# Performance work log

Hardware: AMD Instinct MI355X
Metric: run time of the kernel (lower is better)

The kernel has to match this reference:

```python
import jax, jax.numpy as jnp
import numpy as np

NX, NY, NZ = 432, 496, 1
D = 64        # num_pt_features
K = 3         # NUM_K
M = 1024      # memory size
BEV = 128     # num_bev_features
NCOORD = 3
NV = 10000    # pillars in scene
NP = 16384    # points in scene
BN_EPS = 1e-3
SHRINK = 0.0025


def hard_shrink_relu(x, lambd, eps=1e-12):
    return jax.nn.relu(x - lambd) * x / (jnp.abs(x - lambd) + eps)


def batchnorm_train(x, gamma, beta, eps=BN_EPS):
    # torch BatchNorm1d training-mode math (biased variance)
    mu = jnp.mean(x, axis=0)
    var = jnp.mean((x - mu) ** 2, axis=0)
    return (x - mu) * jax.lax.rsqrt(var + eps) * gamma + beta


def pdist2(a, b, eps=1e-5):
    # sqrt(eps + |  ||a||^2 + ||b||^2 - 2 a.b |), shape [n1, n2]
    n1 = jnp.sum(a * a, axis=1, keepdims=True)
    n2 = jnp.sum(b * b, axis=1, keepdims=True)
    d2 = n1 + n2.T - 2.0 * (a @ b.T)
    return jnp.sqrt(eps + jnp.abs(d2))


def memory_lookup(x_flat, mem_w, shrink):
    # MemAE-style memory unit: softmax addressing + hard shrink + L1 renorm
    att = jax.nn.softmax(x_flat @ mem_w.T, axis=1)          # [N, M]
    att = hard_shrink_relu(att, shrink)
    att = att / jnp.maximum(jnp.sum(jnp.abs(att), axis=1, keepdims=True), 1e-12)
    return att @ mem_w                                       # [N, D]


def setup_inputs() -> dict:
    key = jax.random.key(0)
    ks = jax.random.split(key, 8)
    rng = np.random.default_rng(0)
    flat = rng.choice(NX * NY, size=NV, replace=False)       # unique BEV cells
    x = (flat % NX).astype(np.int32)
    y = (flat // NX).astype(np.int32)
    coords = jnp.asarray(np.stack([np.zeros(NV, np.int32), x, y,
                                   np.zeros(NV, np.int32)], axis=1))  # (b, x, y, z)
    pc = jax.random.uniform(ks[1], (NP, 4), dtype=jnp.float32)
    point_coords = pc * jnp.array([0.0, NX, NY, 1.0], dtype=jnp.float32)
    return {
        "pillar_features": jax.random.normal(ks[0], (NV, D), dtype=jnp.float32),
        "coords": coords,
        "point_features": jax.random.normal(ks[2], (NP, D), dtype=jnp.float32),
        "point_coords": point_coords,
        "adapt_w": jax.random.normal(ks[3], (BEV // 2, D * K), dtype=jnp.float32) * 0.05,
        "bn1_g": jnp.ones((BEV // 2,), dtype=jnp.float32),
        "bn1_b": jnp.zeros((BEV // 2,), dtype=jnp.float32),
        "weight_w": jax.random.normal(ks[4], (2, BEV // 2), dtype=jnp.float32) * 0.1,
        "bn2_g": jnp.ones((2,), dtype=jnp.float32),
        "bn2_b": jnp.zeros((2,), dtype=jnp.float32),
        "mem_w": jax.random.normal(ks[5], (M, D), dtype=jnp.float32) * 0.1,
    }


def reference(pillar_features, coords, point_features, point_coords,
              adapt_w, bn1_g, bn1_b, weight_w, bn2_g, bn2_b, mem_w):
    nv = pillar_features.shape[0]
    pillars = pillar_features.T                              # [D, nv]

    # --- coord-based retrieval: smallest-K pdist(pillar coords, point coords) ---
    dist = pdist2(coords.astype(jnp.float32), point_coords)  # [nv, np]
    _, idx_c = jax.lax.top_k(-dist, K)                       # [nv, K]
    pillars_positive_coord = point_features[idx_c]           # [nv, K, D]

    # --- feature-based retrieval: top-K of softmax(points @ pillars, axis=0) ---
    score = jax.nn.softmax(point_features @ pillars, axis=0) # [np, nv]
    _, idx_f = jax.lax.top_k(score.T, K)                     # [nv, K]
    points_positive = point_features[idx_f]                  # [nv, K, D]

    # --- memory unit on both branches ---
    out_f = memory_lookup(points_positive.reshape(nv * K, D), mem_w, SHRINK).reshape(nv, K * D)
    out_c = memory_lookup(pillars_positive_coord.reshape(nv * K, D), mem_w, SHRINK).reshape(nv, K * D)

    f = jax.nn.relu(batchnorm_train(out_f @ adapt_w.T, bn1_g, bn1_b))  # [nv, 64]
    c = jax.nn.relu(batchnorm_train(out_c @ adapt_w.T, bn1_g, bn1_b))  # [nv, 64]
    w = jax.nn.softmax(batchnorm_train(pillar_features @ weight_w.T, bn2_g, bn2_b), axis=-1)
    pillars_aug = w[:, :1] * f + w[:, 1:2] * c               # [nv, 64]
    pillars_full = jnp.concatenate([pillars, pillars_aug.T], axis=0)  # [128, nv]

    # --- scatter to BEV canvas ---
    bev_idx = coords[:, 1] + coords[:, 2] * NX + coords[:, 3]
    spatial = jnp.zeros((BEV, NX * NY), dtype=pillar_features.dtype).at[:, bev_idx].set(pillars_full)
    pind = jnp.zeros((NCOORD, NX * NY), dtype=pillar_features.dtype)
    pind = pind.at[0, bev_idx].set(coords[:, 2].astype(jnp.float32))
    pind = pind.at[1, bev_idx].set(coords[:, 3].astype(jnp.float32))
    pind = pind.at[2, bev_idx].set(coords[:, 1].astype(jnp.float32))

    spatial_features = spatial.reshape(1, BEV * NZ, NY, NX)
    spatial_indices = pind.reshape(1, NCOORD * NZ, NY, NX)
    return spatial_features, spatial_indices
```

## Files before the change

kernel.cpp:

```cpp
#include <hip/hip_runtime.h>
#include <math.h>

#define NXc 432
#define NYc 496
#define NVc 10000
#define NPc 16384
#define CELLS (NXc*NYc)
#define SHRINKc 0.0025f
#define NVPAD 10048
#define NBX 27
#define NBY 31
#define NBIN (NBX*NBY)

typedef unsigned short u16;
typedef __attribute__((ext_vector_type(8))) short s16x8;
typedef __attribute__((ext_vector_type(4))) float f32x4;

__device__ __forceinline__ unsigned med3u(unsigned a, unsigned b, unsigned c) {
    unsigned d;
    asm("v_med3_u32 %0, %1, %2, %3" : "=v"(d) : "v"(a), "v"(b), "v"(c));
    return d;
}

__device__ __forceinline__ u16 f2b(float x) {
    unsigned u = __float_as_uint(x);
    unsigned r = (u + 0x7fffu + ((u >> 16) & 1u)) >> 16;
    return (u16)r;
}

__global__ __launch_bounds__(256) void k_init(const float* __restrict__ pillar,
                                              const float* __restrict__ pfeat,
                                              const float* __restrict__ memw,
                                              const float* __restrict__ adapt,
                                              float* __restrict__ stats,
                                              int* __restrict__ cellMap,
                                              u16* __restrict__ pillarH,
                                              u16* __restrict__ pfeatH,
                                              u16* __restrict__ memwH,
                                              u16* __restrict__ memwTH,
                                              u16* __restrict__ badaptH) {
    int gid = blockIdx.x * 256 + threadIdx.x;
    if (gid < CELLS) cellMap[gid] = -1;
    if (gid < 260) stats[gid] = 0.f;
    const int N1 = NVPAD * 64;
    const int N2 = N1 + NPc * 64;
    const int N3 = N2 + 65536;
    const int N4 = N3 + 65536;
    if (gid < N1) {
        int v = gid >> 6;
        pillarH[gid] = f2b(v < NVc ? pillar[gid] : 0.f);
    } else if (gid < N2) {
        pfeatH[gid - N1] = f2b(pfeat[gid - N1]);
    } else if (gid < N3) {
        memwH[gid - N2] = f2b(memw[gid - N2]);
    } else if (gid < N4) {
        int i = gid - N3;
        int d = i >> 10, j = i & 1023;
        memwTH[i] = f2b(memw[j * 64 + d]);
    } else {
        int i = gid - N4;
        int c = i >> 6, d = i & 63;
        badaptH[i] = f2b(adapt[(c & 63) * 192 + (c >> 6) * 64 + d]);
    }
}

__global__ __launch_bounds__(1024) void k_pre(const float* __restrict__ pcoord,
                                              int* __restrict__ binStart,
                                              float4* __restrict__ binPC) {
    __shared__ int hcnt[1024];
    __shared__ int sc[1024];
    __shared__ int cur[1024];
    int t = threadIdx.x;
    hcnt[t] = 0;
    __syncthreads();
    for (int j = t; j < NPc; j += 1024) {
        float qx = pcoord[j * 4 + 1], qy = pcoord[j * 4 + 2];
        int bx = (int)(qx * 0.0625f); if (bx > NBX - 1) bx = NBX - 1;
        int by = (int)(qy * 0.0625f); if (by > NBY - 1) by = NBY - 1;
        atomicAdd(&hcnt[by * NBX + bx], 1);
    }
    __syncthreads();
    int vcount = (t < NBIN) ? hcnt[t] : 0;
    sc[t] = vcount;
    __syncthreads();
    for (int off = 1; off < 1024; off <<= 1) {
        int add = (t >= off) ? sc[t - off] : 0;
        __syncthreads();
        sc[t] += add;
        __syncthreads();
    }
    int excl = sc[t] - vcount;
    cur[t] = excl;
    if (t <= NBIN) binStart[t] = excl;
    __syncthreads();
    for (int j = t; j < NPc; j += 1024) {
        float qx = pcoord[j * 4 + 1], qy = pcoord[j * 4 + 2], qz = pcoord[j * 4 + 3];
        int bx = (int)(qx * 0.0625f); if (bx > NBX - 1) bx = NBX - 1;
        int by = (int)(qy * 0.0625f); if (by > NBY - 1) by = NBY - 1;
        int slot = atomicAdd(&cur[by * NBX + bx], 1);
        binPC[slot] = make_float4(qx, qy, qz * qz, __uint_as_float((unsigned)j));
    }
}

__global__ __launch_bounds__(256) void k_fused(const u16* __restrict__ pillarH,
                                               const u16* __restrict__ pfeatH,
                                               const u16* __restrict__ memwH,
                                               const u16* __restrict__ memwTH,
                                               const int* __restrict__ coords,
                                               const float4* __restrict__ binPC,
                                               const int* __restrict__ binStart,
                                               u16* __restrict__ PoutH,
                                               int* __restrict__ dIdx6,
                                               int* __restrict__ sIdx) {
    __shared__ union {
        u16 bf[2][8192];
        struct { u16 wh[4096]; u16 wt[4096]; u16 st[4][1024]; } m;
    } smem;
    int bid = blockIdx.x;
    int t = threadIdx.x;
    int w = t >> 6, l = t & 63;
    int lm = l & 15, qd = l >> 4;

    if (bid < 256) {
        int pb = bid * 64;
        u16* WH = smem.m.wh;
        u16* WT = smem.m.wt;
        u16* ST = &smem.m.st[w][0];
        const u16* arow = pfeatH + (size_t)(pb + 16 * w + lm) * 64 + qd * 8;
        s16x8 a0 = *(const s16x8*)arow;
        s16x8 a1 = *(const s16x8*)(arow + 32);
        float mM[4] = {-INFINITY, -INFINITY, -INFINITY, -INFINITY};
        float Zs[4] = {0.f, 0.f, 0.f, 0.f};
        for (int tile = 0; tile < 16; ++tile) {
            __syncthreads();
#pragma unroll
            for (int r = 0; r < 2; ++r) {
                int q = t + 256 * r;
                int row = q >> 3, g = q & 7;
                uint4 v = *(const uint4*)(memwH + (size_t)(tile * 64 + row) * 64 + g * 8);
                *(uint4*)&WH[(((row >> 4) * 8 + g) * 16 + ((row & 15) ^ g)) * 8] = v;
            }
            __syncthreads();
            f32x4 acc[4];
#pragma unroll
            for (int st = 0; st < 4; ++st) {
                s16x8 b0 = *(const s16x8*)&WH[((st * 8 + qd) * 16 + (lm ^ qd)) * 8];
                s16x8 b1 = *(const s16x8*)&WH[((st * 8 + qd + 4) * 16 + (lm ^ (qd + 4))) * 8];
                f32x4 z = {0.f, 0.f, 0.f, 0.f};
                z = __builtin_amdgcn_mfma_f32_16x16x32_bf16(a0, b0, z, 0, 0, 0);
                z = __builtin_amdgcn_mfma_f32_16x16x32_bf16(a1, b1, z, 0, 0, 0);
                acc[st] = z;
            }
#pragma unroll
            for (int r = 0; r < 4; ++r) {
                float tmax = acc[0][r];
#pragma unroll
                for (int st = 1; st < 4; ++st) tmax = fmaxf(tmax, acc[st][r]);
                float mn = fmaxf(mM[r], tmax);
                float zacc = Zs[r] * __expf(mM[r] - mn);
#pragma unroll
                for (int st = 0; st < 4; ++st) zacc += __expf(acc[st][r] - mn);
                mM[r] = mn; Zs[r] = zacc;
            }
        }
#pragma unroll
        for (int r = 0; r < 4; ++r) {
#pragma unroll
            for (int off = 1; off < 16; off <<= 1) {
                float om = __shfl_xor(mM[r], off);
                float oz = __shfl_xor(Zs[r], off);
                float mn = fmaxf(mM[r], om);
                Zs[r] = Zs[r] * __expf(mM[r] - mn) + oz * __expf(om - mn);
                mM[r] = mn;
            }
        }
        float invZ[4], L1[4] = {0.f, 0.f, 0.f, 0.f};
#pragma unroll
        for (int r = 0; r < 4; ++r) invZ[r] = 1.f / Zs[r];
        f32x4 oacc[4];
#pragma unroll
        for (int n = 0; n < 4; ++n) oacc[n] = (f32x4){0.f, 0.f, 0.f, 0.f};
        for (int tile = 0; tile < 16; ++tile) {
            __syncthreads();
#pragma unroll
            for (int r = 0; r < 2; ++r) {
                int q = t + 256 * r;
                int row = q >> 3, g = q & 7;
                uint4 v = *(const uint4*)(memwH + (size_t)(tile * 64 + row) * 64 + g * 8);
                *(uint4*)&WH[(((row >> 4) * 8 + g) * 16 + ((row & 15) ^ g)) * 8] = v;
            }
#pragma unroll
            for (int r = 0; r < 2; ++r) {
                int q = t + 256 * r;
                int row = q >> 3, g = q & 7;
                uint4 v = *(const uint4*)(memwTH + (size_t)row * 1024 + tile * 64 + g * 8);
                *(uint4*)&WT[(g * 64 + (row ^ g)) * 8] = v;
            }
            __syncthreads();
#pragma unroll
            for (int st = 0; st < 4; ++st) {
                s16x8 b0 = *(const s16x8*)&WH[((st * 8 + qd) * 16 + (lm ^ qd)) * 8];
                s16x8 b1 = *(const s16x8*)&WH[((st * 8 + qd + 4) * 16 + (lm ^ (qd + 4))) * 8];
                f32x4 z = {0.f, 0.f, 0.f, 0.f};
                z = __builtin_amdgcn_mfma_f32_16x16x32_bf16(a0, b0, z, 0, 0, 0);
                z = __builtin_amdgcn_mfma_f32_16x16x32_bf16(a1, b1, z, 0, 0, 0);
                int g2 = st * 2 + (lm >> 3);
#pragma unroll
                for (int r = 0; r < 4; ++r) {
                    float e = __expf(z[r] - mM[r]);
                    float a = e * invZ[r];
                    float tt = a - SHRINKc;
                    float sres = fmaxf(tt, 0.f) * a / (fabsf(tt) + 1e-12f);
                    L1[r] += sres;
                    int rr = qd * 4 + r;
                    ST[(g2 * 16 + (rr ^ g2)) * 8 + (lm & 7)] = f2b(sres);
                }
            }
#pragma unroll
            for (int ks = 0; ks < 2; ++ks) {
                int g = ks * 4 + qd;
                s16x8 af = *(const s16x8*)&ST[(g * 16 + (lm ^ g)) * 8];
#pragma unroll
                for (int n = 0; n < 4; ++n) {
                    s16x8 bf = *(const s16x8*)&WT[(g * 64 + ((n * 16 + lm) ^ g)) * 8];
                    oacc[n] = __builtin_amdgcn_mfma_f32_16x16x32_bf16(af, bf, oacc[n], 0, 0, 0);
                }
            }
        }
#pragma unroll
        for (int r = 0; r < 4; ++r) {
#pragma unroll
            for (int off = 1; off < 16; off <<= 1) L1[r] += __shfl_xor(L1[r], off);
            L1[r] = 1.f / fmaxf(L1[r], 1e-12f);
        }
#pragma unroll
        for (int n = 0; n < 4; ++n)
#pragma unroll
            for (int r = 0; r < 4; ++r)
                PoutH[(size_t)(pb + 16 * w + qd * 4 + r) * 64 + n * 16 + lm] =
                    f2b(oacc[n][r] * L1[r]);
    } else if (bid < 296) {
        int v = (bid - 256) * 256 + t;
        if (v >= NVc) return;
        int xi = coords[v * 4 + 1], yi = coords[v * 4 + 2];
        float x = (float)xi, y = (float)yi;
        int bx = xi >> 4; if (bx > NBX - 1) bx = NBX - 1;
        int by = yi >> 4; if (by > NBY - 1) by = NBY - 1;
        unsigned kk[6] = {~0u, ~0u, ~0u, ~0u, ~0u, ~0u};
        for (int r = 0; r < 32; ++r) {
            int x0 = bx - r, x1 = bx + r, y0 = by - r, y1 = by + r;
            for (int cy = y0; cy <= y1; ++cy) {
                if (cy < 0 || cy > NBY - 1) continue;
                int step = (cy == y0 || cy == y1) ? 1 : (x1 > x0 ? x1 - x0 : 1);
                for (int cx = x0; cx <= x1; cx += step) {
                    if (cx < 0 || cx > NBX - 1) continue;
                    int b = cy * NBX + cx;
                    int s0 = binStart[b], s1 = binStart[b + 1];
                    for (int s = s0; s < s1; ++s) {
                        float4 p = binPC[s];
                        float e1 = x - p.x, e2 = y - p.y;
                        float d2 = fmaf(e1, e1, fmaf(e2, e2, p.z));
                        unsigned tk = (__float_as_uint(d2) & 0xFFFFC000u) | __float_as_uint(p.w);
                        kk[5] = med3u(kk[4], kk[5], tk);
                        kk[4] = med3u(kk[3], kk[4], tk);
                        kk[3] = med3u(kk[2], kk[3], tk);
                        kk[2] = med3u(kk[1], kk[2], tk);
                        kk[1] = med3u(kk[0], kk[1], tk);
                        kk[0] = kk[0] < tk ? kk[0] : tk;
                    }
                }
            }
            if (kk[2] != ~0u) {
                float d3 = __uint_as_float(kk[2] & 0xFFFFC000u);
                if (256.f * (float)(r * r) > d3 * 1.004f + 1e-3f) break;
            }
        }
#pragma unroll
        for (int j2 = 0; j2 < 6; ++j2) dIdx6[v * 6 + j2] = (int)(kk[j2] & 16383u);
    } else {
        int sb = bid - 296;
        int pb = (sb >> 4) * 64;
        int cb = (sb & 15) * 1024;
        const u16* arow = pillarH + (size_t)(pb + 16 * w + lm) * 64 + qd * 8;
        s16x8 a0 = *(const s16x8*)arow;
        s16x8 a1 = *(const s16x8*)(arow + 32);
        int so[4], doff[4];
#pragma unroll
        for (int r = 0; r < 4; ++r) {
            int q = t + 256 * r;
            int row = q >> 3, g = q & 7;
            so[r] = row * 64 + g * 8;
            doff[r] = (((row >> 4) * 8 + g) * 16 + ((row & 15) ^ g)) * 8;
        }
        uint4 pre[4];
        const u16* src = pfeatH + (size_t)cb * 64;
#pragma unroll
        for (int r = 0; r < 4; ++r) pre[r] = *(const uint4*)(src + so[r]);
#pragma unroll
        for (int r = 0; r < 4; ++r) *(uint4*)&smem.bf[0][doff[r]] = pre[r];
        unsigned sk[4][4];
#pragma unroll
        for (int r = 0; r < 4; ++r)
#pragma unroll
            for (int j = 0; j < 4; ++j) sk[r][j] = 0u;
        for (int s = 0; s < 8; ++s) {
            __syncthreads();
            if (s < 7) {
                const u16* s2 = src + (size_t)(s + 1) * 128 * 64;
#pragma unroll
                for (int r = 0; r < 4; ++r) pre[r] = *(const uint4*)(s2 + so[r]);
            }
            const u16* B = &smem.bf[s & 1][0];
#pragma unroll
            for (int pt = 0; pt < 8; ++pt) {
                s16x8 b0 = *(const s16x8*)&B[(((pt * 8 + qd) * 16) + (lm ^ qd)) * 8];
                s16x8 b1 = *(const s16x8*)&B[(((pt * 8 + qd + 4) * 16) + (lm ^ (qd + 4))) * 8];
                f32x4 acc = {256.f, 256.f, 256.f, 256.f};
                acc = __builtin_amdgcn_mfma_f32_16x16x32_bf16(a0, b0, acc, 0, 0, 0);
                acc = __builtin_amdgcn_mfma_f32_16x16x32_bf16(a1, b1, acc, 0, 0, 0);
                unsigned idf = (unsigned)(1023 - (s * 128 + pt * 16 + lm));
#pragma unroll
                for (int r = 0; r < 4; ++r) {
                    unsigned key = (__float_as_uint(acc[r]) & 0xFFFFFC00u) | idf;
                    sk[r][3] = med3u(sk[r][2], sk[r][3], key);
                    sk[r][2] = med3u(sk[r][1], sk[r][2], key);
                    sk[r][1] = med3u(sk[r][0], sk[r][1], key);
                    sk[r][0] = sk[r][0] > key ? sk[r][0] : key;
                }
            }
            if (s < 7) {
#pragma unroll
                for (int r = 0; r < 4; ++r) *(uint4*)&smem.bf[(s + 1) & 1][doff[r]] = pre[r];
            }
        }
#pragma unroll
        for (int off = 1; off < 16; off <<= 1) {
#pragma unroll
            for (int r = 0; r < 4; ++r) {
                unsigned o0 = __shfl_xor(sk[r][0], off);
                unsigned o1 = __shfl_xor(sk[r][1], off);
                unsigned o2 = __shfl_xor(sk[r][2], off);
                unsigned o3 = __shfl_xor(sk[r][3], off);
                sk[r][3] = med3u(sk[r][2], sk[r][3], o0);
                sk[r][2] = med3u(sk[r][1], sk[r][2], o0);
                sk[r][1] = med3u(sk[r][0], sk[r][1], o0);
                sk[r][0] = sk[r][0] > o0 ? sk[r][0] : o0;
                sk[r][3] = med3u(sk[r][2], sk[r][3], o1);
                sk[r][2] = med3u(sk[r][1], sk[r][2], o1);
                sk[r][1] = med3u(sk[r][0], sk[r][1], o1);
                sk[r][0] = sk[r][0] > o1 ? sk[r][0] : o1;
                sk[r][3] = med3u(sk[r][2], sk[r][3], o2);
                sk[r][2] = med3u(sk[r][1], sk[r][2], o2);
                sk[r][1] = med3u(sk[r][0], sk[r][1], o2);
                sk[r][0] = sk[r][0] > o2 ? sk[r][0] : o2;
                sk[r][3] = med3u(sk[r][2], sk[r][3], o3);
                sk[r][2] = med3u(sk[r][1], sk[r][2], o3);
                sk[r][1] = med3u(sk[r][0], sk[r][1], o3);
                sk[r][0] = sk[r][0] > o3 ? sk[r][0] : o3;
            }
        }
        if (lm == 0) {
            int chunk = sb & 15;
#pragma unroll
            for (int r = 0; r < 4; ++r) {
                int gpr = pb + 16 * w + qd * 4 + r;
                if (gpr < NVc) {
                    int4 v;
                    v.x = cb + 1023 - (int)(sk[r][0] & 1023u);
                    v.y = cb + 1023 - (int)(sk[r][1] & 1023u);
                    v.z = cb + 1023 - (int)(sk[r][2] & 1023u);
                    v.w = cb + 1023 - (int)(sk[r][3] & 1023u);
                    *(int4*)&sIdx[(chunk * NVc + gpr) * 4] = v;
                }
            }
        }
    }
}

__global__ __launch_bounds__(256) void k_fused2(const u16* __restrict__ PoutH,
                                                const u16* __restrict__ badaptH,
                                                const float* __restrict__ pillar,
                                                const int* __restrict__ coords,
                                                const float* __restrict__ pfeat,
                                                const float* __restrict__ pcoord,
                                                const int* __restrict__ sIdx,
                                                const int* __restrict__ dIdx6,
                                                float* __restrict__ Q,
                                                int* __restrict__ idx_f,
                                                int* __restrict__ idx_c) {
    __shared__ u16 AD[12288];
    int bid = blockIdx.x;
    int t = threadIdx.x;
    if (bid < 256) {
        int w = t >> 6, l = t & 63;
        int lm = l & 15, qd = l >> 4;
        int pb = bid * 64;
#pragma unroll
        for (int r = 0; r < 6; ++r) {
            int q = t + 256 * r;
            int row = q >> 3, g = q & 7;
            uint4 v = *(const uint4*)(badaptH + (size_t)row * 64 + g * 8);
            *(uint4*)&AD[(((row >> 4) * 8 + g) * 16 + ((row & 15) ^ g)) * 8] = v;
        }
        const u16* arow = PoutH + (size_t)(pb + 16 * w + lm) * 64 + qd * 8;
        s16x8 a0 = *(const s16x8*)arow;
        s16x8 a1 = *(const s16x8*)(arow + 32);
        __syncthreads();
        f32x4 acc[12];
#pragma unroll
        for (int nt = 0; nt < 12; ++nt) {
            s16x8 b0 = *(const s16x8*)&AD[(((nt * 8 + qd) * 16) + (lm ^ qd)) * 8];
            s16x8 b1 = *(const s16x8*)&AD[(((nt * 8 + qd + 4) * 16) + (lm ^ (qd + 4))) * 8];
            f32x4 z = {0.f, 0.f, 0.f, 0.f};
            z = __builtin_amdgcn_mfma_f32_16x16x32_bf16(a0, b0, z, 0, 0, 0);
            z = __builtin_amdgcn_mfma_f32_16x16x32_bf16(a1, b1, z, 0, 0, 0);
            acc[nt] = z;
        }
#pragma unroll
        for (int nt = 0; nt < 12; ++nt)
#pragma unroll
            for (int r = 0; r < 4; ++r)
                Q[(size_t)(pb + 16 * w + qd * 4 + r) * 192 + nt * 16 + lm] = acc[nt][r];
    } else {
        int wv = t >> 6, l = t & 63;
        int v = (bid - 256) * 4 + wv;
        int chunk = l >> 2, slot = l & 3;
        int ps = sIdx[(chunk * NVc + v) * 4 + slot];
        int pd = dIdx6[v * 6 + (l < 6 ? l : 0)];
        double s = 0.0;
#pragma unroll
        for (int i = 0; i < 16; ++i) {
            float4 a = *(const float4*)(pillar + v * 64 + 4 * i);
            float4 b = *(const float4*)(pfeat + ps * 64 + 4 * i);
            s += (double)a.x * (double)b.x + (double)a.y * (double)b.y
               + (double)a.z * (double)b.z + (double)a.w * (double)b.w;
        }
        float4 qc = *(const float4*)(pcoord + pd * 4);
        double db_ = (double)coords[v * 4 + 0] - (double)qc.x;
        double dx_ = (double)coords[v * 4 + 1] - (double)qc.y;
        double dy_ = (double)coords[v * 4 + 2] - (double)qc.z;
        double dz_ = (double)coords[v * 4 + 3] - (double)qc.w;
        double d2 = db_ * db_ + dx_ * dx_ + dy_ * dy_ + dz_ * dz_;
        double sv = s; int sx = ps;
        for (int k = 0; k < 3; ++k) {
            double bv = sv; int bi = sx;
#pragma unroll
            for (int off = 32; off >= 1; off >>= 1) {
                double ov = __shfl_xor(bv, off);
                int    oi = __shfl_xor(bi, off);
                if (ov > bv || (ov == bv && oi < bi)) { bv = ov; bi = oi; }
            }
            if (l == 0) idx_f[v * 3 + k] = bi;
            if (sx == bi) { sv = -INFINITY; sx = 0x7fffffff; }
        }
        double dv = d2; int dx2 = pd;
        for (int k = 0; k < 3; ++k) {
            double bv = dv; int bi = dx2;
#pragma unroll
            for (int off = 32; off >= 1; off >>= 1) {
                double ov = __shfl_xor(bv, off);
                int    oi = __shfl_xor(bi, off);
                if (ov < bv || (ov == bv && oi < bi)) { bv = ov; bi = oi; }
            }
            if (l == 0) idx_c[v * 3 + k] = bi;
            if (dx2 == bi) { dv = INFINITY; dx2 = 0x7fffffff; }
        }
    }
}

__global__ __launch_bounds__(256) void k_gather(const float* __restrict__ Q,
                                                const int* __restrict__ idx_f,
                                                const int* __restrict__ idx_c,
                                                const float* __restrict__ pillar,
                                                const int* __restrict__ coords,
                                                const float* __restrict__ ww,
                                                float* __restrict__ f_pre,
                                                float* __restrict__ c_pre,
                                                float* __restrict__ w_pre,
                                                float* __restrict__ stats,
                                                int* __restrict__ cellMap) {
    __shared__ float red[4][4][64];
    __shared__ float redw[4][4];
    int t = threadIdx.x;
    int wv = t >> 6, l = t & 63;
    int base = blockIdx.x * 40;
    int vend = base + 40;
    if (t < 40) {
        int v = base + t;
        int cell = coords[v * 4 + 1] + coords[v * 4 + 2] * NXc + coords[v * 4 + 3];
        cellMap[cell] = v;
    }
    float fs = 0, fq = 0, cs = 0, cq = 0, ws0 = 0, wq0 = 0, ws1 = 0, wq1 = 0;
    float w0l = ww[l], w1l = ww[64 + l];
    for (int v = base + wv; v < vend; v += 4) {
        int if0 = idx_f[v * 3], if1 = idx_f[v * 3 + 1], if2 = idx_f[v * 3 + 2];
        float f = Q[if0 * 192 + l] + Q[if1 * 192 + 64 + l] + Q[if2 * 192 + 128 + l];
        f_pre[v * 64 + l] = f; fs += f; fq += f * f;
        int ic0 = idx_c[v * 3], ic1 = idx_c[v * 3 + 1], ic2 = idx_c[v * 3 + 2];
        float c = Q[ic0 * 192 + l] + Q[ic1 * 192 + 64 + l] + Q[ic2 * 192 + 128 + l];
        c_pre[v * 64 + l] = c; cs += c; cq += c * c;
        float pv = pillar[v * 64 + l];
        float a0 = pv * w0l, a1 = pv * w1l;
#pragma unroll
        for (int off = 32; off >= 1; off >>= 1) {
            a0 += __shfl_xor(a0, off);
            a1 += __shfl_xor(a1, off);
        }
        if (l == 0) { w_pre[v * 2] = a0; w_pre[v * 2 + 1] = a1; }
        ws0 += a0; wq0 += a0 * a0; ws1 += a1; wq1 += a1 * a1;
    }
    red[0][wv][l] = fs; red[1][wv][l] = fq; red[2][wv][l] = cs; red[3][wv][l] = cq;
    if (l == 0) { redw[wv][0] = ws0; redw[wv][1] = wq0; redw[wv][2] = ws1; redw[wv][3] = wq1; }
    __syncthreads();
    if (wv == 0) {
#pragma unroll
        for (int q = 0; q < 4; ++q) {
            float sum = red[q][0][l] + red[q][1][l] + red[q][2][l] + red[q][3][l];
            atomicAdd(&stats[q * 64 + l], sum);
        }
        if (l < 4) {
            float sum = redw[0][l] + redw[1][l] + redw[2][l] + redw[3][l];
            atomicAdd(&stats[256 + l], sum);
        }
    }
}

__global__ __launch_bounds__(256) void k_out2(const int* __restrict__ cellMap,
                                              const float* __restrict__ pillar,
                                              const float* __restrict__ f_pre,
                                              const float* __restrict__ c_pre,
                                              const float* __restrict__ w_pre,
                                              const float* __restrict__ stats,
                                              const float* __restrict__ g1,
                                              const float* __restrict__ b1,
                                              const float* __restrict__ g2,
                                              const float* __restrict__ b2,
                                              float* __restrict__ out) {
    int c4 = (blockIdx.x * 256 + threadIdx.x) * 4;
    if (c4 >= CELLS) return;
    int4 cm = *(const int4*)(cellMap + c4);
    const float invn = 1.0f / (float)NVc;
    float mw0 = stats[256] * invn, vw0 = stats[257] * invn - mw0 * mw0;
    float mw1 = stats[258] * invn, vw1 = stats[259] * invn - mw1 * mw1;
    float rw0 = rsqrtf(vw0 + 1e-3f), rw1 = rsqrtf(vw1 + 1e-3f);
    float g20 = g2[0], b20 = b2[0], g21 = g2[1], b21 = b2[1];
    float w0c[4], w1c[4];
    int cms[4] = {cm.x, cm.y, cm.z, cm.w};
#pragma unroll
    for (int k = 0; k < 4; ++k) {
        int c = cms[k];
        if (c >= 0) {
            float z0 = (w_pre[c * 2] - mw0) * rw0 * g20 + b20;
            float z1 = (w_pre[c * 2 + 1] - mw1) * rw1 * g21 + b21;
            float mz = fmaxf(z0, z1);
            float e0 = __expf(z0 - mz), e1 = __expf(z1 - mz);
            float wd = 1.f / (e0 + e1);
            w0c[k] = e0 * wd; w1c[k] = e1 * wd;
        } else { w0c[k] = 0.f; w1c[k] = 0.f; }
    }
    int f0 = blockIdx.y * 33;
    int f1 = f0 + 33; if (f1 > 131) f1 = 131;
    for (int f = f0; f < f1; ++f) {
        float4 val;
        if (f < 64) {
            val.x = cm.x >= 0 ? pillar[cm.x * 64 + f] : 0.f;
            val.y = cm.y >= 0 ? pillar[cm.y * 64 + f] : 0.f;
            val.z = cm.z >= 0 ? pillar[cm.z * 64 + f] : 0.f;
            val.w = cm.w >= 0 ? pillar[cm.w * 64 + f] : 0.f;
        } else if (f < 128) {
            int fa = f - 64;
            float mf = stats[fa] * invn;
            float rf = rsqrtf(stats[64 + fa] * invn - mf * mf + 1e-3f);
            float mc = stats[128 + fa] * invn;
            float rc = rsqrtf(stats[192 + fa] * invn - mc * mc + 1e-3f);
            float gg = g1[fa], bb = b1[fa];
            float* vv = (float*)&val;
#pragma unroll
            for (int k = 0; k < 4; ++k) {
                int c = cms[k];
                if (c >= 0) {
                    float fv = fmaxf((f_pre[c * 64 + fa] - mf) * rf * gg + bb, 0.f);
                    float cv = fmaxf((c_pre[c * 64 + fa] - mc) * rc * gg + bb, 0.f);
                    vv[k] = w0c[k] * fv + w1c[k] * cv;
                } else vv[k] = 0.f;
            }
        } else if (f == 128) {
            val.x = cm.x >= 0 ? (float)((c4 + 0) / NXc) : 0.f;
            val.y = cm.y >= 0 ? (float)((c4 + 1) / NXc) : 0.f;
            val.z = cm.z >= 0 ? (float)((c4 + 2) / NXc) : 0.f;
            val.w = cm.w >= 0 ? (float)((c4 + 3) / NXc) : 0.f;
        } else if (f == 129) {
            val = make_float4(0.f, 0.f, 0.f, 0.f);
        } else {
            val.x = cm.x >= 0 ? (float)((c4 + 0) % NXc) : 0.f;
            val.y = cm.y >= 0 ? (float)((c4 + 1) % NXc) : 0.f;
            val.z = cm.z >= 0 ? (float)((c4 + 2) % NXc) : 0.f;
            val.w = cm.w >= 0 ? (float)((c4 + 3) % NXc) : 0.f;
        }
        *(float4*)(out + (size_t)f * CELLS + c4) = val;
    }
}

extern "C" void kernel_launch(void* const* d_in, const int* in_sizes, int n_in,
                              void* d_out, int out_size, void* d_ws, size_t ws_size,
                              hipStream_t stream) {
    const float* pillar = (const float*)d_in[0];
    const int*   coords = (const int*)d_in[1];
    const float* pfeat  = (const float*)d_in[2];
    const float* pcoord = (const float*)d_in[3];
    const float* adapt  = (const float*)d_in[4];
    const float* bn1g   = (const float*)d_in[5];
    const float* bn1b   = (const float*)d_in[6];
    const float* ww     = (const float*)d_in[7];
    const float* bn2g   = (const float*)d_in[8];
    const float* bn2b   = (const float*)d_in[9];
    const float* memw   = (const float*)d_in[10];
    float* out = (float*)d_out;
    float* ws  = (float*)d_ws;
    u16*   PoutH = (u16*)(ws + 0);
    float* Q     = ws + 1048576;
    int*   sIdx  = (int*)(ws + 4194304);
    int*   binStart  = (int*)(ws + 4834304);
    int*   dIdx6     = (int*)(ws + 4836824);
    float4* binPC    = (float4*)(ws + 4896824);
    u16*   memwH   = (u16*)(ws + 4970000);
    u16*   memwTH  = (u16*)(ws + 5002768);
    u16*   badaptH = (u16*)(ws + 5035536);
    int*   idxf  = (int*)(ws + 5474304);
    int*   idxc  = (int*)(ws + 5504304);
    float* fpre  = ws + 5534304;
    float* cpre  = ws + 6174304;
    float* wpre  = ws + 6814304;
    float* stats = ws + 6834304;
    int*   cellMap = (int*)(ws + 6840000);
    u16* pillarH = (u16*)(ws + 5534304);
    u16* pfeatH  = pillarH + (size_t)NVPAD * 64;

    k_init  <<<7168, 256, 0, stream>>>(pillar, pfeat, memw, adapt, stats, cellMap,
                                       pillarH, pfeatH, memwH, memwTH, badaptH);
    k_pre   <<<1, 1024, 0, stream>>>(pcoord, binStart, binPC);
    k_fused <<<2808, 256, 0, stream>>>(pillarH, pfeatH, memwH, memwTH, coords,
                                       binPC, binStart, PoutH, dIdx6, sIdx);
    k_fused2<<<2756, 256, 0, stream>>>(PoutH, badaptH, pillar, coords, pfeat, pcoord,
                                       sIdx, dIdx6, Q, idxf, idxc);
    k_gather<<<250, 256, 0, stream>>>(Q, idxf, idxc, pillar, coords, ww,
                                      fpre, cpre, wpre, stats, cellMap);
    k_out2  <<<dim3(210, 4), 256, 0, stream>>>(cellMap, pillar, fpre, cpre, wpre, stats,
                                               bn1g, bn1b, bn2g, bn2b, out);
}
```

Before: 323.7 us.

## Merge point-binning kernel into init kernel as an extra block

Folds the single-block k_pre point-binning pass into k_init as one extra 1024-thread block, so binning runs alongside the bf16 conversion and canvas init instead of as a separate serial launch. k_init's block size changes from 256 to 1024 threads, and point coordinates are now read as one float4 load. The v_med3_u32 inline asm is replaced with plain C min/max, which may compile to more instructions. The risk is that the lone serial binning block becomes the tail of the merged kernel, and the larger blocks may change occupancy.

Result: no change. 320.1 us (-1.1%).

```diff
diff --git a/kernel.cpp b/kernel.cpp
--- a/kernel.cpp
+++ b/kernel.cpp
@@ -17,9 +17,10 @@
 typedef __attribute__((ext_vector_type(4))) float f32x4;
 
 __device__ __forceinline__ unsigned med3u(unsigned a, unsigned b, unsigned c) {
-    unsigned d;
-    asm("v_med3_u32 %0, %1, %2, %3" : "=v"(d) : "v"(a), "v"(b), "v"(c));
-    return d;
+    unsigned mn = a < b ? a : b;
+    unsigned mx = a > b ? a : b;
+    unsigned m2 = mx < c ? mx : c;
+    return mn > m2 ? mn : m2;
 }
 
 __device__ __forceinline__ u16 f2b(float x) {
@@ -28,77 +29,79 @@
     return (u16)r;
 }
 
-__global__ __launch_bounds__(256) void k_init(const float* __restrict__ pillar,
-                                              const float* __restrict__ pfeat,
-                                              const float* __restrict__ memw,
-                                              const float* __restrict__ adapt,
-                                              float* __restrict__ stats,
-                                              int* __restrict__ cellMap,
-                                              u16* __restrict__ pillarH,
-                                              u16* __restrict__ pfeatH,
-                                              u16* __restrict__ memwH,
-                                              u16* __restrict__ memwTH,
-                                              u16* __restrict__ badaptH) {
-    int gid = blockIdx.x * 256 + threadIdx.x;
-    if (gid < CELLS) cellMap[gid] = -1;
-    if (gid < 260) stats[gid] = 0.f;
-    const int N1 = NVPAD * 64;
-    const int N2 = N1 + NPc * 64;
-    const int N3 = N2 + 65536;
-    const int N4 = N3 + 65536;
-    if (gid < N1) {
-        int v = gid >> 6;
-        pillarH[gid] = f2b(v < NVc ? pillar[gid] : 0.f);
-    } else if (gid < N2) {
-        pfeatH[gid - N1] = f2b(pfeat[gid - N1]);
-    } else if (gid < N3) {
-        memwH[gid - N2] = f2b(memw[gid - N2]);
-    } else if (gid < N4) {
-        int i = gid - N3;
-        int d = i >> 10, j = i & 1023;
-        memwTH[i] = f2b(memw[j * 64 + d]);
-    } else {
-        int i = gid - N4;
-        int c = i >> 6, d = i & 63;
-        badaptH[i] = f2b(adapt[(c & 63) * 192 + (c >> 6) * 64 + d]);
-    }
-}
-
-__global__ __launch_bounds__(1024) void k_pre(const float* __restrict__ pcoord,
-                                              int* __restrict__ binStart,
-                                              float4* __restrict__ binPC) {
+__global__ __launch_bounds__(1024) void k_init(const float* __restrict__ pillar,
+                                               const float* __restrict__ pfeat,
+                                               const float* __restrict__ memw,
+                                               const float* __restrict__ adapt,
+                                               const float* __restrict__ pcoord,
+                                               float* __restrict__ stats,
+                                               int* __restrict__ cellMap,
+                                               u16* __restrict__ pillarH,
+                                               u16* __restrict__ pfeatH,
+                                               u16* __restrict__ memwH,
+                                               u16* __restrict__ memwTH,
+                                               u16* __restrict__ badaptH,
+                                               int* __restrict__ binStart,
+                                               float4* __restrict__ binPC) {
     __shared__ int hcnt[1024];
     __shared__ int sc[1024];
     __shared__ int cur[1024];
+    int bid = blockIdx.x;
     int t = threadIdx.x;
-    hcnt[t] = 0;
-    __syncthreads();
-    for (int j = t; j < NPc; j += 1024) {
-        float qx = pcoord[j * 4 + 1], qy = pcoord[j * 4 + 2];
-        int bx = (int)(qx * 0.0625f); if (bx > NBX - 1) bx = NBX - 1;
-        int by = (int)(qy * 0.0625f); if (by > NBY - 1) by = NBY - 1;
-        atomicAdd(&hcnt[by * NBX + bx], 1);
-    }
-    __syncthreads();
-    int vcount = (t < NBIN) ? hcnt[t] : 0;
-    sc[t] = vcount;
-    __syncthreads();
-    for (int off = 1; off < 1024; off <<= 1) {
-        int add = (t >= off) ? sc[t - off] : 0;
+    if (bid < 1792) {
+        int gid = bid * 1024 + t;
+        if (gid < CELLS) cellMap[gid] = -1;
+        if (gid < 260) stats[gid] = 0.f;
+        const int N1 = NVPAD * 64;
+        const int N2 = N1 + NPc * 64;
+        const int N3 = N2 + 65536;
+        const int N4 = N3 + 65536;
+        if (gid < N1) {
+            int v = gid >> 6;
+            pillarH[gid] = f2b(v < NVc ? pillar[gid] : 0.f);
+        } else if (gid < N2) {
+            pfeatH[gid - N1] = f2b(pfeat[gid - N1]);
+        } else if (gid < N3) {
+            memwH[gid - N2] = f2b(memw[gid - N2]);
+        } else if (gid < N4) {
+            int i = gid - N3;
+            int d = i >> 10, j = i & 1023;
+            memwTH[i] = f2b(memw[j * 64 + d]);
+        } else {
+            int i = gid - N4;
+            int c = i >> 6, d = i & 63;
+            badaptH[i] = f2b(adapt[(c & 63) * 192 + (c >> 6) * 64 + d]);
+        }
+    } else {
+        hcnt[t] = 0;
         __syncthreads();
-        sc[t] += add;
+        for (int j = t; j < NPc; j += 1024) {
+            float4 pc = *(const float4*)(pcoord + j * 4);
+            int bx = (int)(pc.y * 0.0625f); if (bx > NBX - 1) bx = NBX - 1;
+            int by = (int)(pc.z * 0.0625f); if (by > NBY - 1) by = NBY - 1;
+            atomicAdd(&hcnt[by * NBX + bx], 1);
+        }
         __syncthreads();
-    }
-    int excl = sc[t] - vcount;
-    cur[t] = excl;
-    if (t <= NBIN) binStart[t] = excl;
-    __syncthreads();
-    for (int j = t; j < NPc; j += 1024) {
-        float qx = pcoord[j * 4 + 1], qy = pcoord[j * 4 + 2], qz = pcoord[j * 4 + 3];
-        int bx = (int)(qx * 0.0625f); if (bx > NBX - 1) bx = NBX - 1;
-        int by = (int)(qy * 0.0625f); if (by > NBY - 1) by = NBY - 1;
-        int slot = atomicAdd(&cur[by * NBX + bx], 1);
-        binPC[slot] = make_float4(qx, qy, qz * qz, __uint_as_float((unsigned)j));
+        int vcount = (t < NBIN) ? hcnt[t] : 0;
+        sc[t] = vcount;
+        __syncthreads();
+        for (int off = 1; off < 1024; off <<= 1) {
+            int add = (t >= off) ? sc[t - off] : 0;
+            __syncthreads();
+            sc[t] += add;
+            __syncthreads();
+        }
+        int excl = sc[t] - vcount;
+        cur[t] = excl;
+        if (t <= NBIN) binStart[t] = excl;
+        __syncthreads();
+        for (int j = t; j < NPc; j += 1024) {
+            float4 pc = *(const float4*)(pcoord + j * 4);
+            int bx = (int)(pc.y * 0.0625f); if (bx > NBX - 1) bx = NBX - 1;
+            int by = (int)(pc.z * 0.0625f); if (by > NBY - 1) by = NBY - 1;
+            int slot = atomicAdd(&cur[by * NBX + bx], 1);
+            binPC[slot] = make_float4(pc.y, pc.z, pc.w * pc.w, __uint_as_float((unsigned)j));
+        }
     }
 }
 
@@ -636,9 +639,9 @@
     u16* pillarH = (u16*)(ws + 5534304);
     u16* pfeatH  = pillarH + (size_t)NVPAD * 64;
 
-    k_init  <<<7168, 256, 0, stream>>>(pillar, pfeat, memw, adapt, stats, cellMap,
-                                       pillarH, pfeatH, memwH, memwTH, badaptH);
-    k_pre   <<<1, 1024, 0, stream>>>(pcoord, binStart, binPC);
+    k_init  <<<1793, 1024, 0, stream>>>(pillar, pfeat, memw, adapt, pcoord, stats, cellMap,
+                                        pillarH, pfeatH, memwH, memwTH, badaptH,
+                                        binStart, binPC);
     k_fused <<<2808, 256, 0, stream>>>(pillarH, pfeatH, memwH, memwTH, coords,
                                        binPC, binStart, PoutH, dIdx6, sIdx);
     k_fused2<<<2756, 256, 0, stream>>>(PoutH, badaptH, pillar, coords, pfeat, pcoord,
```
